# Kernel tuning notes

Hardware: AMD Instinct MI355X
Metric: run time of the kernel (lower is better)

## Reference

```python
import jax, jax.numpy as jnp
import numpy as np

N, DIM = 100000, 512
HID = DIM // 2


def _mlp(z, W1, b1, W2, b2):
    # shared scorer: [N, dim] -> [N, 1]
    h = jax.nn.relu(z @ W1 + b1)
    return h @ W2 + b2


def setup_inputs() -> dict:
    key = jax.random.key(0)
    k1, k2, k3, k4 = jax.random.split(key, 4)
    s1 = 1.0 / np.sqrt(DIM)
    s2 = 1.0 / np.sqrt(HID)
    return {
        "z1": jax.random.normal(k1, (N, DIM), dtype=jnp.float32),
        "z2": jax.random.normal(k2, (N, DIM), dtype=jnp.float32),
        "W1": jax.random.normal(k3, (DIM, HID), dtype=jnp.float32) * s1,
        "b1": jnp.zeros((HID,), dtype=jnp.float32),
        "W2": jax.random.normal(k4, (HID, 1), dtype=jnp.float32) * s2,
        "b2": jnp.zeros((1,), dtype=jnp.float32),
    }


def reference(z1, z2, W1, b1, W2, b2):
    x = _mlp(z1, W1, b1, W2, b2)  # [N, 1]
    y = _mlp(z2, W1, b1, W2, b2)  # [N, 1]
    # exp-normalize pair: score_x = e^x / (e^x + e^y) == sigmoid(x - y)
    # computed exactly as in the original (plain exp, no max-subtract)
    e_x = jnp.exp(x)
    e_y = jnp.exp(y)
    denom = e_x + e_y
    score_x = e_x / denom  # [N, 1]
    score_y = e_y / denom  # [N, 1]
    # diag(score) @ z  ==  score * z  (row-wise broadcast scale)
    return score_x * z1 + score_y * z2
```

## Files before the change

### kernel.cpp

```cpp
#include <hip/hip_runtime.h>
#include <hip/hip_bf16.h>
#include <cmath>

#define DIM 512
#define HID 256
#define NW 12
#define TILES 6
#define ROWS_PB 96
#define NCHUNK 8
#define CHUNK_BYTES 32768
#define ROUNDS 32

typedef __attribute__((ext_vector_type(8))) short short8;
typedef __attribute__((ext_vector_type(4))) float f32x4;

__device__ __forceinline__ unsigned short f2bf(float f) {
  union { float f; unsigned u; } v; v.f = f;
  unsigned u = v.u;
  return (unsigned short)((u + 0x7FFFu + ((u >> 16) & 1u)) >> 16);
}

__global__ void w1_swz_kernel(const float* __restrict__ W1,
                              unsigned short* __restrict__ w1s) {
  int tid = blockIdx.x * blockDim.x + threadIdx.x;
  if (tid >= DIM * HID) return;
  int k = tid / HID;
  int c = tid - k * HID;
  w1s[(((k >> 3) * HID) + c) * 8 + (k & 7)] = f2bf(W1[tid]);
}

__device__ __forceinline__ short8 cvt8(const f32x4 p0, const f32x4 p1) {
  short8 r;
  r[0] = (short)f2bf(p0[0]); r[1] = (short)f2bf(p0[1]);
  r[2] = (short)f2bf(p0[2]); r[3] = (short)f2bf(p0[3]);
  r[4] = (short)f2bf(p1[0]); r[5] = (short)f2bf(p1[1]);
  r[6] = (short)f2bf(p1[2]); r[7] = (short)f2bf(p1[3]);
  return r;
}

__global__ __launch_bounds__(768, 3) void fa_main_kernel(
    const float* __restrict__ z1, const float* __restrict__ z2,
    const unsigned short* __restrict__ w1s,
    const float* __restrict__ b1, const float* __restrict__ W2,
    const float* __restrict__ b2, float* __restrict__ out, int n) {
  __shared__ unsigned short Bs[2][CHUNK_BYTES / 2];

  const int t = threadIdx.x;
  const int w = t >> 6;
  const int l = t & 63;
  const int l15 = l & 15, l16 = l >> 4;
  const int src = (w >= TILES) ? 1 : 0;
  const int tile = src ? (w - TILES) : w;
  const int row0 = blockIdx.x * ROWS_PB;
  const int myrow = row0 + tile * 16 + l15;
  const bool rok = myrow < n;
  const float* zz = src ? z2 : z1;
  const float* ap = zz + (size_t)myrow * DIM + (l16 << 3);
  const f32x4 zf4 = (f32x4){0.f, 0.f, 0.f, 0.f};

  {
    const char* gsrc = (const char*)w1s + l * 16;
    for (int r = w; r < ROUNDS; r += NW)
      __builtin_amdgcn_global_load_lds(
          (const __attribute__((address_space(1))) void*)(gsrc + r * 1024),
          (__attribute__((address_space(3))) void*)((char*)&Bs[0][0] + r * 1024),
          16, 0, 0);
  }
  f32x4 pa[4];
#pragma unroll
  for (int q = 0; q < 4; ++q)
    pa[q] = rok ? *(const f32x4*)(ap + ((q >> 1) << 5) + ((q & 1) << 2)) : zf4;

  f32x4 acc[16];
#pragma unroll
  for (int f = 0; f < 16; ++f) acc[f] = zf4;

  __syncthreads();

#pragma unroll 2
  for (int c = 0; c < NCHUNK; ++c) {
    const int cur = c & 1;
    if (c + 1 < NCHUNK) {
      const char* gsrc = (const char*)w1s + (c + 1) * CHUNK_BYTES + l * 16;
      for (int r = w; r < ROUNDS; r += NW)
        __builtin_amdgcn_global_load_lds(
            (const __attribute__((address_space(1))) void*)(gsrc + r * 1024),
            (__attribute__((address_space(3))) void*)((char*)&Bs[cur ^ 1][0] +
                                                      r * 1024),
            16, 0, 0);
    }
    f32x4 na[4];
    if (c + 1 < NCHUNK) {
      const float* apn = ap + ((c + 1) << 6);
#pragma unroll
      for (int q = 0; q < 4; ++q)
        na[q] = rok ? *(const f32x4*)(apn + ((q >> 1) << 5) + ((q & 1) << 2))
                    : zf4;
    }
#pragma unroll
    for (int s = 0; s < 2; ++s) {
      const short8 af = cvt8(pa[(s << 1)], pa[(s << 1) + 1]);
      const short8* bp =
          (const short8*)&Bs[cur][0] + (((s << 2) + l16) << 8) + l15;
#pragma unroll
      for (int f = 0; f < 16; ++f) {
        const short8 bf = bp[f << 4];
        acc[f] =
            __builtin_amdgcn_mfma_f32_16x16x32_bf16(af, bf, acc[f], 0, 0, 0);
      }
    }
    if (c + 1 < NCHUNK) {
#pragma unroll
      for (int q = 0; q < 4; ++q) pa[q] = na[q];
    }
    __syncthreads();
  }

  float part[4] = {0.f, 0.f, 0.f, 0.f};
#pragma unroll
  for (int f = 0; f < 16; ++f) {
    const int cc = (f << 4) + l15;
    const float w2v = W2[cc];
    const float b1v = b1[cc];
#pragma unroll
    for (int r = 0; r < 4; ++r) {
      const float h = acc[f][r] + b1v;
      part[r] += (h > 0.f) ? h * w2v : 0.f;
    }
  }
#pragma unroll
  for (int r = 0; r < 4; ++r) {
#pragma unroll
    for (int m = 1; m < 16; m <<= 1) part[r] += __shfl_xor(part[r], m, 16);
  }
  float* xs = (float*)&Bs[0][0];
  if (l15 == 0) {
#pragma unroll
    for (int r = 0; r < 4; ++r)
      xs[src * ROWS_PB + tile * 16 + (l16 << 2) + r] = part[r];
  }
  __syncthreads();

#pragma unroll 1
  for (int r = 0; r < 16; ++r) {
    const int rl = tile * 16 + r;
    const int grow = row0 + rl;
    if (grow < n) {
      const float d = xs[ROWS_PB + rl] - xs[rl];
      const float sx = 1.f / (1.f + __expf(d));
      const float sy = 1.f - sx;
      const size_t off = (size_t)grow * DIM + (src << 8) + (l << 2);
      const f32x4 a4 = *(const f32x4*)(z1 + off);
      const f32x4 b4 = *(const f32x4*)(z2 + off);
      f32x4 o;
      o[0] = sx * a4[0] + sy * b4[0];
      o[1] = sx * a4[1] + sy * b4[1];
      o[2] = sx * a4[2] + sy * b4[2];
      o[3] = sx * a4[3] + sy * b4[3];
      *(f32x4*)(out + off) = o;
    }
  }
}

extern "C" void kernel_launch(void* const* d_in, const int* in_sizes, int n_in,
                              void* d_out, int out_size, void* d_ws,
                              size_t ws_size, hipStream_t stream) {
  const float* z1 = (const float*)d_in[0];
  const float* z2 = (const float*)d_in[1];
  const float* W1 = (const float*)d_in[2];
  const float* b1 = (const float*)d_in[3];
  const float* W2 = (const float*)d_in[4];
  const float* b2 = (const float*)d_in[5];
  float* out = (float*)d_out;
  const int n = in_sizes[0] / DIM;
  unsigned short* w1s = (unsigned short*)d_ws;

  hipLaunchKernelGGL(w1_swz_kernel, dim3((DIM * HID + 255) / 256), dim3(256),
                     0, stream, W1, w1s);
  const int nwg = (n + ROWS_PB - 1) / ROWS_PB;
  hipLaunchKernelGGL(fa_main_kernel, dim3(nwg), dim3(768), 0, stream, z1, z2,
                     w1s, b1, W2, b2, out, n);
}
```

Before: 213.0 us.

## Shrink workgroups to 32 rows with smaller W1 chunks and dedicated score buffer

Cuts the workgroup from 12 waves and 96 rows to 4 waves and 32 rows, and halves the K-chunk of W1 staged in LDS per iteration, which doubles the number of chunk iterations. Each wave now processes one K-slice per chunk. A separate shared array holds the per-row scores. The aim is more workgroups and better occupancy and balance across CUs. In exchange, each block reloads the full W1 for far fewer rows, which raises L2/LDS traffic for W1 and adds more barriers per row.

```diff
diff --git a/kernel.cpp b/kernel.cpp
--- a/kernel.cpp
+++ b/kernel.cpp
@@ -4,12 +4,9 @@
 
 #define DIM 512
 #define HID 256
-#define NW 12
-#define TILES 6
-#define ROWS_PB 96
-#define NCHUNK 8
-#define CHUNK_BYTES 32768
-#define ROUNDS 32
+#define ROWS_PB 32
+#define NCHUNK 16
+#define CB 16384
 
 typedef __attribute__((ext_vector_type(8))) short short8;
 typedef __attribute__((ext_vector_type(4))) float f32x4;
@@ -38,20 +35,22 @@
   return r;
 }
 
-__global__ __launch_bounds__(768, 3) void fa_main_kernel(
+__global__ __launch_bounds__(256, 4) void fa_main_kernel(
     const float* __restrict__ z1, const float* __restrict__ z2,
     const unsigned short* __restrict__ w1s,
     const float* __restrict__ b1, const float* __restrict__ W2,
     const float* __restrict__ b2, float* __restrict__ out, int n) {
-  __shared__ unsigned short Bs[2][CHUNK_BYTES / 2];
+  __shared__ unsigned short Bs[2][CB / 2];
+  __shared__ float xs[2][ROWS_PB];
 
   const int t = threadIdx.x;
   const int w = t >> 6;
   const int l = t & 63;
   const int l15 = l & 15, l16 = l >> 4;
-  const int src = (w >= TILES) ? 1 : 0;
-  const int tile = src ? (w - TILES) : w;
+  const int src = w & 1;
+  const int tile = w >> 1;
   const int row0 = blockIdx.x * ROWS_PB;
+  if (row0 >= n) return;
   const int myrow = row0 + tile * 16 + l15;
   const bool rok = myrow < n;
   const float* zz = src ? z2 : z1;
@@ -60,16 +59,15 @@
 
   {
     const char* gsrc = (const char*)w1s + l * 16;
-    for (int r = w; r < ROUNDS; r += NW)
+#pragma unroll
+    for (int r = w; r < 16; r += 4)
       __builtin_amdgcn_global_load_lds(
           (const __attribute__((address_space(1))) void*)(gsrc + r * 1024),
           (__attribute__((address_space(3))) void*)((char*)&Bs[0][0] + r * 1024),
           16, 0, 0);
   }
-  f32x4 pa[4];
-#pragma unroll
-  for (int q = 0; q < 4; ++q)
-    pa[q] = rok ? *(const f32x4*)(ap + ((q >> 1) << 5) + ((q & 1) << 2)) : zf4;
+  f32x4 pa0 = rok ? *(const f32x4*)(ap) : zf4;
+  f32x4 pa1 = rok ? *(const f32x4*)(ap + 4) : zf4;
 
   f32x4 acc[16];
 #pragma unroll
@@ -77,42 +75,31 @@
 
   __syncthreads();
 
-#pragma unroll 2
   for (int c = 0; c < NCHUNK; ++c) {
     const int cur = c & 1;
+    f32x4 na0 = zf4, na1 = zf4;
     if (c + 1 < NCHUNK) {
-      const char* gsrc = (const char*)w1s + (c + 1) * CHUNK_BYTES + l * 16;
-      for (int r = w; r < ROUNDS; r += NW)
+      const char* gsrc = (const char*)w1s + (c + 1) * CB + l * 16;
+#pragma unroll
+      for (int r = w; r < 16; r += 4)
         __builtin_amdgcn_global_load_lds(
             (const __attribute__((address_space(1))) void*)(gsrc + r * 1024),
             (__attribute__((address_space(3))) void*)((char*)&Bs[cur ^ 1][0] +
                                                       r * 1024),
             16, 0, 0);
+      const float* apn = ap + ((c + 1) << 5);
+      na0 = rok ? *(const f32x4*)(apn) : zf4;
+      na1 = rok ? *(const f32x4*)(apn + 4) : zf4;
     }
-    f32x4 na[4];
-    if (c + 1 < NCHUNK) {
-      const float* apn = ap + ((c + 1) << 6);
+    const short8 af = cvt8(pa0, pa1);
+    const short8* bp = (const short8*)&Bs[cur][0] + (l16 << 8) + l15;
 #pragma unroll
-      for (int q = 0; q < 4; ++q)
-        na[q] = rok ? *(const f32x4*)(apn + ((q >> 1) << 5) + ((q & 1) << 2))
-                    : zf4;
+    for (int f = 0; f < 16; ++f) {
+      const short8 bf = bp[f << 4];
+      acc[f] = __builtin_amdgcn_mfma_f32_16x16x32_bf16(af, bf, acc[f], 0, 0, 0);
     }
-#pragma unroll
-    for (int s = 0; s < 2; ++s) {
-      const short8 af = cvt8(pa[(s << 1)], pa[(s << 1) + 1]);
-      const short8* bp =
-          (const short8*)&Bs[cur][0] + (((s << 2) + l16) << 8) + l15;
-#pragma unroll
-      for (int f = 0; f < 16; ++f) {
-        const short8 bf = bp[f << 4];
-        acc[f] =
-            __builtin_amdgcn_mfma_f32_16x16x32_bf16(af, bf, acc[f], 0, 0, 0);
-      }
-    }
-    if (c + 1 < NCHUNK) {
-#pragma unroll
-      for (int q = 0; q < 4; ++q) pa[q] = na[q];
-    }
+    pa0 = na0;
+    pa1 = na1;
     __syncthreads();
   }
 
@@ -133,23 +120,23 @@
 #pragma unroll
     for (int m = 1; m < 16; m <<= 1) part[r] += __shfl_xor(part[r], m, 16);
   }
-  float* xs = (float*)&Bs[0][0];
   if (l15 == 0) {
 #pragma unroll
     for (int r = 0; r < 4; ++r)
-      xs[src * ROWS_PB + tile * 16 + (l16 << 2) + r] = part[r];
+      xs[src][tile * 16 + (l16 << 2) + r] = part[r];
   }
   __syncthreads();
 
+  const int colh = src << 8;
 #pragma unroll 1
   for (int r = 0; r < 16; ++r) {
     const int rl = tile * 16 + r;
     const int grow = row0 + rl;
     if (grow < n) {
-      const float d = xs[ROWS_PB + rl] - xs[rl];
+      const float d = xs[1][rl] - xs[0][rl];
       const float sx = 1.f / (1.f + __expf(d));
       const float sy = 1.f - sx;
-      const size_t off = (size_t)grow * DIM + (src << 8) + (l << 2);
+      const size_t off = (size_t)grow * DIM + colh + (l << 2);
       const f32x4 a4 = *(const f32x4*)(z1 + off);
       const f32x4 b4 = *(const f32x4*)(z2 + off);
       f32x4 o;
@@ -178,6 +165,6 @@
   hipLaunchKernelGGL(w1_swz_kernel, dim3((DIM * HID + 255) / 256), dim3(256),
                      0, stream, W1, w1s);
   const int nwg = (n + ROWS_PB - 1) / ROWS_PB;
-  hipLaunchKernelGGL(fa_main_kernel, dim3(nwg), dim3(768), 0, stream, z1, z2,
+  hipLaunchKernelGGL(fa_main_kernel, dim3(nwg), dim3(256), 0, stream, z1, z2,
                      w1s, b1, W2, b2, out, n);
 }
```

Result: no change. 211.8 us (-0.5%).
